# Kernel tuning notes

Hardware: AMD Instinct MI355X
Metric: run time of the kernel (lower is better)

Reference implementation:

```python
import jax, jax.numpy as jnp
import numpy as np

D = 128          # embedding dim
N_INIT = 100000  # number of initial (axiom) clauses
L = 64           # topological levels of derived clauses
M = 4096         # derived clauses per level
N_THAX = 2000    # distinct axiom-name (thax) embeddings
N_SINE = 32      # sine-level embeddings
N_RULES = 256    # distinct inference rules (each with its own 2-ary MLP)
N_TOT = N_INIT + L * M


def setup_inputs() -> dict:
    key = jax.random.key(0)
    ks = jax.random.split(key, 10)
    rng = np.random.default_rng(0)
    # parents of level-l nodes point to any node created strictly earlier
    parents = np.stack(
        [rng.integers(0, N_INIT + l * M, size=(M, 2)) for l in range(L)]
    ).astype(np.int32)  # [L, M, 2]
    return {
        "thax_table": jax.random.normal(ks[0], (N_THAX, D), jnp.float32) * 0.1,
        "sine_table": jax.random.normal(ks[1], (N_SINE, D), jnp.float32) * 0.1,
        "rule_W": jax.random.normal(ks[2], (N_RULES, 2 * D, D), jnp.float32) * (1.0 / np.sqrt(2 * D)),
        "rule_b": jax.random.normal(ks[3], (N_RULES, D), jnp.float32) * 0.01,
        "eval_w": jax.random.normal(ks[4], (D,), jnp.float32) * (1.0 / np.sqrt(D)),
        "eval_b": jax.random.normal(ks[5], (1,), jnp.float32) * 0.01,
        "pos_vals": jax.random.uniform(ks[6], (N_TOT,), jnp.float32, 0.01, 1.0),
        "neg_vals": jax.random.uniform(ks[7], (N_TOT,), jnp.float32, 0.01, 1.0),
        "init_thax": jax.random.randint(ks[8], (N_INIT,), 0, N_THAX, jnp.int32),
        "init_sine": jax.random.randint(ks[9], (N_INIT,), 0, N_SINE, jnp.int32),
        "parents": jnp.asarray(parents),
        "rules": jnp.asarray(rng.integers(0, N_RULES, size=(L, M)).astype(np.int32)),
    }


def reference(thax_table, sine_table, rule_W, rule_b, eval_w, eval_b,
              pos_vals, neg_vals, init_thax, init_sine, parents, rules):
    n_init = init_thax.shape[0]
    n_lvl, m = rules.shape
    d = thax_table.shape[1]

    # init nodes: embed = init_embeds[thax]() + sine_embedder(sine)
    init_emb = thax_table[init_thax] + sine_table[init_sine]  # [N_INIT, D]
    store0 = jnp.concatenate(
        [init_emb, jnp.zeros((n_lvl * m, d), init_emb.dtype)], axis=0)  # [N_TOT, D]

    # deriv nodes, level by level: gather 2 parents, per-rule MLP (cat -> Linear -> ReLU)
    def step(store, xs):
        lvl, par, rul = xs                       # par: [M,2] int, rul: [M] int
        pe = store[par].reshape(m, 2 * d)        # gather parent embeddings
        emb = jax.nn.relu(jnp.einsum('mi,mio->mo', pe, rule_W[rul]) + rule_b[rul])
        store = jax.lax.dynamic_update_slice(store, emb, (n_init + lvl * m, 0))
        return store, None

    store, _ = jax.lax.scan(step, store0, (jnp.arange(n_lvl), parents, rules))

    # eval_net + weighted BCEWithLogits (pos_weight = tot_neg / tot_pos)
    logits = store @ eval_w + eval_b[0]          # [N_TOT]
    tot = pos_vals + neg_vals
    y = pos_vals / tot
    pw = jnp.sum(neg_vals) / jnp.sum(pos_vals)
    per_node = pw * y * jax.nn.softplus(-logits) + (1.0 - y) * jax.nn.softplus(logits)
    loss = jnp.sum(tot * per_node).reshape(1)
    posOK = jnp.sum(jnp.where(logits >= 0.0, pos_vals, 0.0))
    negOK = jnp.sum(jnp.where(logits < 0.0, neg_vals, 0.0))
    return (loss, posOK, negOK)
```

## Files before the change

### kernel.cpp

```cpp
#include <hip/hip_runtime.h>

#define D      128
#define NINIT  100000
#define LVLS   64
#define M      4096
#define NRULES 256
#define NTOT   (NINIT + LVLS * M)
#define NTHR   512
#define TILE   32

typedef __attribute__((ext_vector_type(8))) short short8;
typedef __attribute__((ext_vector_type(4))) float floatx4;

#define ST_OFF 256
#define SI_OFF (ST_OFF + (size_t)NTOT * D * 2)
#define RO_OFF (SI_OFF + (size_t)LVLS * M * 4)
#define FL_OFF (RO_OFF + (size_t)LVLS * (NRULES + 1) * 4)

#define CBAR() asm volatile("" ::: "memory")

__device__ __forceinline__ unsigned short f2bf(float x) {
  unsigned u = __float_as_uint(x);
  u += 0x7fffu + ((u >> 16) & 1u);
  return (unsigned short)(u >> 16);
}

__device__ __forceinline__ float softplusf(float x) {
  return fmaxf(x, 0.f) + log1pf(expf(-fabsf(x)));
}

__device__ __forceinline__ void st_sys(unsigned* p, unsigned v) {
  __hip_atomic_store(p, v, __ATOMIC_RELAXED, __HIP_MEMORY_SCOPE_SYSTEM);
}
__device__ __forceinline__ void st_sys64(unsigned long long* p,
                                         unsigned long long v) {
  __hip_atomic_store(p, v, __ATOMIC_RELAXED, __HIP_MEMORY_SCOPE_SYSTEM);
}
__device__ __forceinline__ unsigned ld_sys(const unsigned* p) {
  return __hip_atomic_load(p, __ATOMIC_RELAXED, __HIP_MEMORY_SCOPE_SYSTEM);
}
__device__ __forceinline__ void wait_flag(const unsigned* f) {
  int guard = 1 << 17;
  while (__builtin_expect(ld_sys(f) == 0u, 0) && --guard)
    __builtin_amdgcn_s_sleep(1);
  CBAR();
}

__device__ __forceinline__ void gbar_light(unsigned* bcnt, unsigned* bgen) {
  __syncthreads();
  if (threadIdx.x == 0) {
    unsigned g = ld_sys(bgen);
    unsigned v = __hip_atomic_fetch_add(bcnt, 1u, __ATOMIC_RELAXED,
                                        __HIP_MEMORY_SCOPE_SYSTEM);
    if (v == gridDim.x - 1) {
      st_sys(bcnt, 0u);
      st_sys(bgen, g + 1u);
    } else {
      int guard = 1 << 22;
      while (ld_sys(bgen) == g && --guard) __builtin_amdgcn_s_sleep(2);
    }
  }
  __syncthreads();
}

__device__ __forceinline__ bool adv_cursor(int r, const int* __restrict__ ro,
                                           int& l, int& t0, int& off, int& cnt) {
  t0 += TILE;
  while (t0 >= cnt) {
    if (++l >= LVLS) return false;
    off = ro[l * (NRULES + 1) + r];
    cnt = ro[l * (NRULES + 1) + r + 1] - off;
    t0 = 0;
  }
  return true;
}

__global__ __launch_bounds__(NTHR, 2) void fused_kernel(
    const float* __restrict__ thax_table, const float* __restrict__ sine_table,
    const float* __restrict__ rule_W, const float* __restrict__ rule_b,
    const float* __restrict__ eval_w, const float* __restrict__ eval_b,
    const float* __restrict__ pos, const float* __restrict__ neg,
    const int* __restrict__ init_thax, const int* __restrict__ init_sine,
    const int* __restrict__ parents,
    const int* __restrict__ rules,
    unsigned short* __restrict__ store, int* __restrict__ sorted_idx,
    int* __restrict__ rule_off, unsigned* __restrict__ flags,
    float* __restrict__ sums, unsigned* __restrict__ bvars,
    float* __restrict__ out) {
  __shared__ unsigned short pe[TILE * 264];
  __shared__ unsigned short ot[TILE * 136];
  __shared__ int s_sid[2][TILE];
  __shared__ int s_cnt[NRULES];
  __shared__ int s_base[NRULES + 1];
  __shared__ float racc[4];

  unsigned* bcnt = bvars;
  unsigned* bgen = bvars + 1;

  const int r = blockIdx.x;
  const int tid = threadIdx.x;
  const int wave = tid >> 6, lane = tid & 63;
  const int col = (wave << 4) + (lane & 15);
  const int node = tid >> 4;
  const int segq = tid & 15;
  const int gid = r * NTHR + tid;
  const int gthreads = NRULES * NTHR;

  float aP1 = 0.f, aP2 = 0.f, a_pos = 0.f, a_neg = 0.f;
  const float eb = eval_b[0];
  float w8[8];
  {
    float4 wA = ((const float4*)eval_w)[segq * 2];
    float4 wB = ((const float4*)eval_w)[segq * 2 + 1];
    w8[0] = wA.x; w8[1] = wA.y; w8[2] = wA.z; w8[3] = wA.w;
    w8[4] = wB.x; w8[5] = wB.y; w8[6] = wB.z; w8[7] = wB.w;
  }

  short8 bf[8];
  {
    const float* Wr = rule_W + (size_t)r * (2 * D * D);
    const int krow_base = (lane >> 4) * 8;
#pragma unroll
    for (int ks = 0; ks < 8; ++ks) {
      union { short8 s; unsigned short us[8]; } c;
#pragma unroll
      for (int j = 0; j < 8; ++j)
        c.us[j] = f2bf(Wr[(size_t)(ks * 32 + krow_base + j) * D + col]);
      bf[ks] = c.s;
    }
  }
  const float bias = rule_b[r * D + col];

  if (r < LVLS) {
    const int l = r;
    const int* rl = rules + (size_t)l * M;
    if (tid < NRULES) s_cnt[tid] = 0;
    __syncthreads();
    for (int m = tid; m < M; m += NTHR) atomicAdd(&s_cnt[rl[m]], 1);
    __syncthreads();
    if (tid == 0) {
      int run = 0;
      for (int q = 0; q < NRULES; ++q) { s_base[q] = run; run += s_cnt[q]; }
      s_base[NRULES] = run;
    }
    __syncthreads();
    if (tid < NRULES) {
      st_sys((unsigned*)&rule_off[(size_t)l * (NRULES + 1) + tid],
             (unsigned)s_base[tid]);
      s_cnt[tid] = s_base[tid];
    }
    if (tid == 0)
      st_sys((unsigned*)&rule_off[(size_t)l * (NRULES + 1) + NRULES],
             (unsigned)M);
    __syncthreads();
    for (int m = tid; m < M; m += NTHR) {
      int p = atomicAdd(&s_cnt[rl[m]], 1);
      st_sys((unsigned*)&sorted_idx[(size_t)l * M + p], (unsigned)m);
    }
  }

  for (int idx = gid; idx < NINIT * 16; idx += gthreads) {
    int nd = idx >> 4, sg = idx & 15;
    const float4* t = (const float4*)(thax_table + (size_t)init_thax[nd] * D) + sg * 2;
    const float4* s = (const float4*)(sine_table + (size_t)init_sine[nd] * D) + sg * 2;
    float4 a0 = t[0], a1 = t[1], b0 = s[0], b1 = s[1];
    float v[8] = {a0.x + b0.x, a0.y + b0.y, a0.z + b0.z, a0.w + b0.w,
                  a1.x + b1.x, a1.y + b1.y, a1.z + b1.z, a1.w + b1.w};
    unsigned p0 = (unsigned)f2bf(v[0]) | ((unsigned)f2bf(v[1]) << 16);
    unsigned p1 = (unsigned)f2bf(v[2]) | ((unsigned)f2bf(v[3]) << 16);
    unsigned p2 = (unsigned)f2bf(v[4]) | ((unsigned)f2bf(v[5]) << 16);
    unsigned p3 = (unsigned)f2bf(v[6]) | ((unsigned)f2bf(v[7]) << 16);
    unsigned long long* dst =
        (unsigned long long*)(store + (size_t)nd * D + sg * 8);
    st_sys64(dst + 0, (unsigned long long)p0 | ((unsigned long long)p1 << 32));
    st_sys64(dst + 1, (unsigned long long)p2 | ((unsigned long long)p3 << 32));

    float pd = v[0] * w8[0] + v[1] * w8[1] + v[2] * w8[2] + v[3] * w8[3] +
               v[4] * w8[4] + v[5] * w8[5] + v[6] * w8[6] + v[7] * w8[7];
    pd += __shfl_xor(pd, 1, 64);
    pd += __shfl_xor(pd, 2, 64);
    pd += __shfl_xor(pd, 4, 64);
    pd += __shfl_xor(pd, 8, 64);
    if (sg == 0) {
      float logit = pd + eb;
      float pp = pos[nd], nn = neg[nd];
      float tot = pp + nn, y = pp / tot;
      aP1 += tot * y * softplusf(-logit);
      aP2 += tot * (1.f - y) * softplusf(logit);
      if (logit >= 0.f) a_pos += pp; else a_neg += nn;
    }
  }

  {
    float sp = 0.f, sn = 0.f;
    for (int i = gid; i < NTOT; i += gthreads) {
      sp += pos[i];
      sn += neg[i];
    }
    for (int m = 32; m; m >>= 1) {
      sp += __shfl_xor(sp, m, 64);
      sn += __shfl_xor(sn, m, 64);
    }
    if (lane == 0) {
      atomicAdd(&sums[0], sp);
      atomicAdd(&sums[1], sn);
    }
  }

  gbar_light(bcnt, bgen);

  const float pw = sums[1] / sums[0];

  int lL = -1, t0L = 0, offL = 0, cntL = 0;

  bool validA = adv_cursor(r, rule_off, lL, t0L, offL, cntL);
  int lA = lL, t0A = t0L, cntA = cntL;
  int parA0 = 0, parA1 = 0;
  bool lateA0 = false, lateA1 = false;
  unsigned reA0 = 1u, reA1 = 1u;
  float pPosA = 0.f, pNegA = 0.f;
  uint4 gA0 = {0, 0, 0, 0}, gA1 = {0, 0, 0, 0};
  if (validA) {
    int gj = t0A + node; if (gj > cntA - 1) gj = cntA - 1;
    int sid = sorted_idx[(size_t)lA * M + offL + gj];
    parA0 = parents[((size_t)lA * M + sid) * 2 + 0];
    parA1 = parents[((size_t)lA * M + sid) * 2 + 1];
    pPosA = pos[NINIT + lA * M + sid];
    pNegA = neg[NINIT + lA * M + sid];
    if (parA0 >= NINIT) wait_flag(flags + (parA0 - NINIT));
    if (parA1 >= NINIT) wait_flag(flags + (parA1 - NINIT));
    gA0 = *(const uint4*)(store + (size_t)parA0 * D + segq * 8);
    gA1 = *(const uint4*)(store + (size_t)parA1 * D + segq * 8);
    if (segq == 0) s_sid[0][node] = sid;
  }

  bool validB = validA && adv_cursor(r, rule_off, lL, t0L, offL, cntL);
  int lB = lL, t0B = t0L, cntB = cntL;
  int sidB = 0, parB0 = 0, parB1 = 0;
  unsigned fB0 = 1u, fB1 = 1u;
  if (validB) {
    int gj = t0B + node; if (gj > cntB - 1) gj = cntB - 1;
    sidB = sorted_idx[(size_t)lB * M + offL + gj];
    parB0 = parents[((size_t)lB * M + sidB) * 2 + 0];
    parB1 = parents[((size_t)lB * M + sidB) * 2 + 1];
    fB0 = parB0 >= NINIT ? ld_sys(flags + (parB0 - NINIT)) : 1u;
    fB1 = parB1 >= NINIT ? ld_sys(flags + (parB1 - NINIT)) : 1u;
  }

  bool validC = validB && adv_cursor(r, rule_off, lL, t0L, offL, cntL);
  int lC = lL, t0C = t0L, cntC = cntL;
  int sidC = 0, parC0 = 0, parC1 = 0;
  if (validC) {
    int gj = t0C + node; if (gj > cntC - 1) gj = cntC - 1;
    sidC = sorted_idx[(size_t)lC * M + offL + gj];
    parC0 = parents[((size_t)lC * M + sidC) * 2 + 0];
    parC1 = parents[((size_t)lC * M + sidC) * 2 + 1];
  }

  bool validD = validC && adv_cursor(r, rule_off, lL, t0L, offL, cntL);
  int lD = lL, t0D = t0L, offD = offL, cntD = cntL;

  int p = 0;
  while (validA) {
    if (lateA0 || lateA1) {
      bool n0 = lateA0 && (reA0 == 0u);
      bool n1 = lateA1 && (reA1 == 0u);
      if (n0 || n1) {
        int guard = 1 << 17;
        while (guard--) {
          unsigned f0 = n0 ? ld_sys(flags + (parA0 - NINIT)) : 1u;
          unsigned f1 = n1 ? ld_sys(flags + (parA1 - NINIT)) : 1u;
          if (f0 != 0u && f1 != 0u) break;
          __builtin_amdgcn_s_sleep(1);
        }
      }
      CBAR();
      if (lateA0) gA0 = *(const uint4*)(store + (size_t)parA0 * D + segq * 8);
      if (lateA1) gA1 = *(const uint4*)(store + (size_t)parA1 * D + segq * 8);
    }

    *(uint4*)(pe + node * 264 + segq * 8) = gA0;
    *(uint4*)(pe + node * 264 + 128 + segq * 8) = gA1;
    __syncthreads();
    if (validB && segq == 0) s_sid[p ^ 1][node] = sidB;

    floatx4 acc0 = {0.f, 0.f, 0.f, 0.f}, acc1 = {0.f, 0.f, 0.f, 0.f};
#pragma unroll
    for (int ks = 0; ks < 8; ++ks) {
      short8 a0 = *(const short8*)(pe + (lane & 15) * 264 + ks * 32 + (lane >> 4) * 8);
      short8 a1 = *(const short8*)(pe + (16 + (lane & 15)) * 264 + ks * 32 + (lane >> 4) * 8);
      acc0 = __builtin_amdgcn_mfma_f32_16x16x32_bf16(a0, bf[ks], acc0, 0, 0, 0);
      acc1 = __builtin_amdgcn_mfma_f32_16x16x32_bf16(a1, bf[ks], acc1, 0, 0, 0);
    }
#pragma unroll
    for (int reg = 0; reg < 4; ++reg) {
      int row = (lane >> 4) * 4 + reg;
      float v0 = acc0[reg] + bias;
      float v1 = acc1[reg] + bias;
      ot[row * 136 + col] = f2bf(v0 > 0.f ? v0 : 0.f);
      ot[(16 + row) * 136 + col] = f2bf(v1 > 0.f ? v1 : 0.f);
    }
    __syncthreads();

    {
      const int n_baseA = NINIT + lA * M;
      int nsid[4]; bool inr[4]; int S = 0;
#pragma unroll
      for (int k = 0; k < 4; ++k) {
        int nd = wave + 8 * k;
        nsid[k] = s_sid[p][nd];
        inr[k] = (t0A + nd) < cntA;
        if (inr[k]) {
          st_sys((unsigned*)(store + (size_t)(n_baseA + nsid[k]) * D) + lane,
                 *(const unsigned*)(ot + nd * 136 + lane * 2));
          ++S;
        }
      }
      CBAR();
#pragma unroll
      for (int k = 0; k < 4; ++k) {
        if (inr[k]) {
          if (S == 4)      asm volatile("s_waitcnt vmcnt(3)" ::: "memory");
          else if (S == 3) asm volatile("s_waitcnt vmcnt(2)" ::: "memory");
          else if (S == 2) asm volatile("s_waitcnt vmcnt(1)" ::: "memory");
          else             asm volatile("s_waitcnt vmcnt(0)" ::: "memory");
          if (lane == 0) st_sys(flags + lA * M + nsid[k], 1u);
        }
      }
      CBAR();
    }

    bool lateB0 = validB && parB0 >= NINIT && fB0 == 0u;
    bool lateB1 = validB && parB1 >= NINIT && fB1 == 0u;
    uint4 gB0, gB1;
    {
      const unsigned short* a0 =
          (validB && !lateB0) ? store + (size_t)parB0 * D : store;
      const unsigned short* a1 =
          (validB && !lateB1) ? store + (size_t)parB1 * D : store;
      gB0 = *(const uint4*)(a0 + segq * 8);
      gB1 = *(const uint4*)(a1 + segq * 8);
    }
    float pPosB = 0.f, pNegB = 0.f;
    if (validB) {
      pPosB = pos[NINIT + lB * M + sidB];
      pNegB = neg[NINIT + lB * M + sidB];
    }
    int sidD = 0, parD0 = 0, parD1 = 0;
    if (validD) {
      int gj = t0D + node; if (gj > cntD - 1) gj = cntD - 1;
      sidD = sorted_idx[(size_t)lD * M + offD + gj];
      parD0 = parents[((size_t)lD * M + sidD) * 2 + 0];
      parD1 = parents[((size_t)lD * M + sidD) * 2 + 1];
    }
    unsigned fC0 = 1u, fC1 = 1u;
    if (validC) {
      fC0 = ld_sys(flags + (parC0 >= NINIT ? parC0 - NINIT : 0));
      fC1 = ld_sys(flags + (parC1 >= NINIT ? parC1 - NINIT : 0));
      if (parC0 < NINIT) fC0 = 1u;
      if (parC1 < NINIT) fC1 = 1u;
    }
    unsigned reB0 = 1u, reB1 = 1u;
    if (lateB0) reB0 = ld_sys(flags + (parB0 - NINIT));
    if (lateB1) reB1 = ld_sys(flags + (parB1 - NINIT));
    CBAR();

    {
      const uint4 u = *(const uint4*)(ot + node * 136 + segq * 8);
      float pd = __uint_as_float(u.x << 16) * w8[0] +
                 __uint_as_float(u.x & 0xffff0000u) * w8[1] +
                 __uint_as_float(u.y << 16) * w8[2] +
                 __uint_as_float(u.y & 0xffff0000u) * w8[3] +
                 __uint_as_float(u.z << 16) * w8[4] +
                 __uint_as_float(u.z & 0xffff0000u) * w8[5] +
                 __uint_as_float(u.w << 16) * w8[6] +
                 __uint_as_float(u.w & 0xffff0000u) * w8[7];
      pd += __shfl_xor(pd, 1, 64);
      pd += __shfl_xor(pd, 2, 64);
      pd += __shfl_xor(pd, 4, 64);
      pd += __shfl_xor(pd, 8, 64);
      if (segq == 0 && (t0A + node) < cntA) {
        float logit = pd + eb;
        float tot = pPosA + pNegA, y = pPosA / tot;
        aP1 += tot * y * softplusf(-logit);
        aP2 += tot * (1.f - y) * softplusf(logit);
        if (logit >= 0.f) a_pos += pPosA; else a_neg += pNegA;
      }
    }

    gA0 = gB0; gA1 = gB1; lateA0 = lateB0; lateA1 = lateB1;
    reA0 = reB0; reA1 = reB1;
    parA0 = parB0; parA1 = parB1;
    pPosA = pPosB; pNegA = pNegB;
    lA = lB; t0A = t0B; cntA = cntB; validA = validB;
    sidB = sidC; parB0 = parC0; parB1 = parC1; fB0 = fC0; fB1 = fC1;
    lB = lC; t0B = t0C; cntB = cntC; validB = validC;
    sidC = sidD; parC0 = parD0; parC1 = parD1;
    lC = lD; t0C = t0D; cntC = cntD; validC = validD;
    validD = validC && adv_cursor(r, rule_off, lL, t0L, offL, cntL);
    lD = lL; t0D = t0L; offD = offL; cntD = cntL;
    p ^= 1;
  }

  for (int m = 32; m; m >>= 1) {
    aP1   += __shfl_xor(aP1,   m, 64);
    aP2   += __shfl_xor(aP2,   m, 64);
    a_pos += __shfl_xor(a_pos, m, 64);
    a_neg += __shfl_xor(a_neg, m, 64);
  }
  if (tid == 0) { racc[0] = 0.f; racc[1] = 0.f; racc[2] = 0.f; racc[3] = 0.f; }
  __syncthreads();
  if (lane == 0) {
    atomicAdd(&racc[0], aP1);
    atomicAdd(&racc[1], aP2);
    atomicAdd(&racc[2], a_pos);
    atomicAdd(&racc[3], a_neg);
  }
  __syncthreads();
  if (tid == 0) {
    atomicAdd(&out[0], pw * racc[0] + racc[1]);
    atomicAdd(&out[1], racc[2]);
    atomicAdd(&out[2], racc[3]);
  }
}

extern "C" void kernel_launch(void* const* d_in, const int* in_sizes, int n_in,
                              void* d_out, int out_size, void* d_ws, size_t ws_size,
                              hipStream_t stream) {
  const float* thax_table = (const float*)d_in[0];
  const float* sine_table = (const float*)d_in[1];
  const float* rule_W     = (const float*)d_in[2];
  const float* rule_b     = (const float*)d_in[3];
  const float* eval_w     = (const float*)d_in[4];
  const float* eval_b     = (const float*)d_in[5];
  const float* pos_vals   = (const float*)d_in[6];
  const float* neg_vals   = (const float*)d_in[7];
  const int*   init_thax  = (const int*)d_in[8];
  const int*   init_sine  = (const int*)d_in[9];
  const int*   parents    = (const int*)d_in[10];
  const int*   rules      = (const int*)d_in[11];

  float* out = (float*)d_out;
  char* ws = (char*)d_ws;
  float* sums = (float*)ws;
  unsigned* bvars = (unsigned*)(ws + 128);
  unsigned short* store = (unsigned short*)(ws + ST_OFF);
  int* sorted_idx = (int*)(ws + SI_OFF);
  int* rule_off   = (int*)(ws + RO_OFF);
  unsigned* flags = (unsigned*)(ws + FL_OFF);

  (void)hipMemsetAsync(d_out, 0, 3 * sizeof(float), stream);
  (void)hipMemsetAsync(d_ws, 0, 256, stream);
  (void)hipMemsetAsync(ws + FL_OFF, 0, (size_t)LVLS * M * 4, stream);

  void* args[] = {&thax_table, &sine_table, &rule_W, &rule_b, &eval_w, &eval_b,
                  &pos_vals, &neg_vals, &init_thax, &init_sine, &parents,
                  &rules, &store, &sorted_idx, &rule_off, &flags, &sums,
                  &bvars, &out};
  (void)hipLaunchCooperativeKernel((void*)fused_kernel, dim3(NRULES),
                                   dim3(NTHR), args, 0, stream);
}
```

Measured before the change: 419.8 us.

## Deepen software pipeline, batch flag waits, parallel scan, split init work off level blocks

Lengthens the per-block prefetch pipeline by one stage so sorted indices, parents, pos/neg values and flag polls are issued further ahead. Flag publication is deferred until after the eval dot product, using a single vmcnt wait, instead of being interleaved with per-store waits. Spin waits now poll both parent flags together with wave-wide __all checks and no sleep. The serial rule-count prefix sum becomes a parallel scan, and init-embedding and pos/neg sum work is moved to the blocks that do not sort levels. The goal is to hide gather and flag latency on the dependent level chain, at the cost of more registers and busier polling.

```diff
diff --git a/kernel.cpp b/kernel.cpp
--- a/kernel.cpp
+++ b/kernel.cpp
@@ -39,10 +39,20 @@
 __device__ __forceinline__ unsigned ld_sys(const unsigned* p) {
   return __hip_atomic_load(p, __ATOMIC_RELAXED, __HIP_MEMORY_SCOPE_SYSTEM);
 }
-__device__ __forceinline__ void wait_flag(const unsigned* f) {
-  int guard = 1 << 17;
-  while (__builtin_expect(ld_sys(f) == 0u, 0) && --guard)
-    __builtin_amdgcn_s_sleep(1);
+
+__device__ __forceinline__ void wait2(const unsigned* f0, bool n0,
+                                      const unsigned* f1, bool n1) {
+  if (__all(!(n0 || n1))) return;
+  unsigned a0 = ld_sys(f0), a1 = ld_sys(f1);
+  int guard = 1 << 16;
+  for (;;) {
+    unsigned b0 = ld_sys(f0), b1 = ld_sys(f1);
+    bool ok = (!n0 || a0 != 0u) && (!n1 || a1 != 0u);
+    if (__all(ok) || !--guard) break;
+    a0 = ld_sys(f0); a1 = ld_sys(f1);
+    ok = (!n0 || b0 != 0u) && (!n1 || b1 != 0u);
+    if (__all(ok) || !--guard) break;
+  }
   CBAR();
 }
 
@@ -103,8 +113,6 @@
   const int col = (wave << 4) + (lane & 15);
   const int node = tid >> 4;
   const int segq = tid & 15;
-  const int gid = r * NTHR + tid;
-  const int gthreads = NRULES * NTHR;
 
   float aP1 = 0.f, aP2 = 0.f, a_pos = 0.f, a_neg = 0.f;
   const float eb = eval_b[0];
@@ -138,16 +146,20 @@
     __syncthreads();
     for (int m = tid; m < M; m += NTHR) atomicAdd(&s_cnt[rl[m]], 1);
     __syncthreads();
-    if (tid == 0) {
-      int run = 0;
-      for (int q = 0; q < NRULES; ++q) { s_base[q] = run; run += s_cnt[q]; }
-      s_base[NRULES] = run;
-    }
-    __syncthreads();
+    int c = (tid < NRULES) ? s_cnt[tid] : 0;
+    if (tid < NRULES) s_base[tid] = c;
+    __syncthreads();
+    for (int off = 1; off < NRULES; off <<= 1) {
+      int t = (tid < NRULES && tid >= off) ? s_base[tid - off] : 0;
+      __syncthreads();
+      if (tid < NRULES) s_base[tid] += t;
+      __syncthreads();
+    }
     if (tid < NRULES) {
+      int ex = s_base[tid] - c;
       st_sys((unsigned*)&rule_off[(size_t)l * (NRULES + 1) + tid],
-             (unsigned)s_base[tid]);
-      s_cnt[tid] = s_base[tid];
+             (unsigned)ex);
+      s_cnt[tid] = ex;
     }
     if (tid == 0)
       st_sys((unsigned*)&rule_off[(size_t)l * (NRULES + 1) + NRULES],
@@ -157,43 +169,42 @@
       int p = atomicAdd(&s_cnt[rl[m]], 1);
       st_sys((unsigned*)&sorted_idx[(size_t)l * M + p], (unsigned)m);
     }
-  }
-
-  for (int idx = gid; idx < NINIT * 16; idx += gthreads) {
-    int nd = idx >> 4, sg = idx & 15;
-    const float4* t = (const float4*)(thax_table + (size_t)init_thax[nd] * D) + sg * 2;
-    const float4* s = (const float4*)(sine_table + (size_t)init_sine[nd] * D) + sg * 2;
-    float4 a0 = t[0], a1 = t[1], b0 = s[0], b1 = s[1];
-    float v[8] = {a0.x + b0.x, a0.y + b0.y, a0.z + b0.z, a0.w + b0.w,
-                  a1.x + b1.x, a1.y + b1.y, a1.z + b1.z, a1.w + b1.w};
-    unsigned p0 = (unsigned)f2bf(v[0]) | ((unsigned)f2bf(v[1]) << 16);
-    unsigned p1 = (unsigned)f2bf(v[2]) | ((unsigned)f2bf(v[3]) << 16);
-    unsigned p2 = (unsigned)f2bf(v[4]) | ((unsigned)f2bf(v[5]) << 16);
-    unsigned p3 = (unsigned)f2bf(v[6]) | ((unsigned)f2bf(v[7]) << 16);
-    unsigned long long* dst =
-        (unsigned long long*)(store + (size_t)nd * D + sg * 8);
-    st_sys64(dst + 0, (unsigned long long)p0 | ((unsigned long long)p1 << 32));
-    st_sys64(dst + 1, (unsigned long long)p2 | ((unsigned long long)p3 << 32));
-
-    float pd = v[0] * w8[0] + v[1] * w8[1] + v[2] * w8[2] + v[3] * w8[3] +
-               v[4] * w8[4] + v[5] * w8[5] + v[6] * w8[6] + v[7] * w8[7];
-    pd += __shfl_xor(pd, 1, 64);
-    pd += __shfl_xor(pd, 2, 64);
-    pd += __shfl_xor(pd, 4, 64);
-    pd += __shfl_xor(pd, 8, 64);
-    if (sg == 0) {
-      float logit = pd + eb;
-      float pp = pos[nd], nn = neg[nd];
-      float tot = pp + nn, y = pp / tot;
-      aP1 += tot * y * softplusf(-logit);
-      aP2 += tot * (1.f - y) * softplusf(logit);
-      if (logit >= 0.f) a_pos += pp; else a_neg += nn;
-    }
-  }
-
-  {
+  } else {
+    const int gid3 = (r - LVLS) * NTHR + tid;
+    const int gstride3 = (NRULES - LVLS) * NTHR;
+    for (int idx = gid3; idx < NINIT * 16; idx += gstride3) {
+      int nd = idx >> 4, sg = idx & 15;
+      const float4* t = (const float4*)(thax_table + (size_t)init_thax[nd] * D) + sg * 2;
+      const float4* s = (const float4*)(sine_table + (size_t)init_sine[nd] * D) + sg * 2;
+      float4 a0 = t[0], a1 = t[1], b0 = s[0], b1 = s[1];
+      float v[8] = {a0.x + b0.x, a0.y + b0.y, a0.z + b0.z, a0.w + b0.w,
+                    a1.x + b1.x, a1.y + b1.y, a1.z + b1.z, a1.w + b1.w};
+      unsigned p0 = (unsigned)f2bf(v[0]) | ((unsigned)f2bf(v[1]) << 16);
+      unsigned p1 = (unsigned)f2bf(v[2]) | ((unsigned)f2bf(v[3]) << 16);
+      unsigned p2 = (unsigned)f2bf(v[4]) | ((unsigned)f2bf(v[5]) << 16);
+      unsigned p3 = (unsigned)f2bf(v[6]) | ((unsigned)f2bf(v[7]) << 16);
+      unsigned long long* dst =
+          (unsigned long long*)(store + (size_t)nd * D + sg * 8);
+      st_sys64(dst + 0, (unsigned long long)p0 | ((unsigned long long)p1 << 32));
+      st_sys64(dst + 1, (unsigned long long)p2 | ((unsigned long long)p3 << 32));
+
+      float pd = v[0] * w8[0] + v[1] * w8[1] + v[2] * w8[2] + v[3] * w8[3] +
+                 v[4] * w8[4] + v[5] * w8[5] + v[6] * w8[6] + v[7] * w8[7];
+      pd += __shfl_xor(pd, 1, 64);
+      pd += __shfl_xor(pd, 2, 64);
+      pd += __shfl_xor(pd, 4, 64);
+      pd += __shfl_xor(pd, 8, 64);
+      if (sg == 0) {
+        float logit = pd + eb;
+        float pp = pos[nd], nn = neg[nd];
+        float tot = pp + nn, y = pp / tot;
+        aP1 += tot * y * softplusf(-logit);
+        aP2 += tot * (1.f - y) * softplusf(logit);
+        if (logit >= 0.f) a_pos += pp; else a_neg += nn;
+      }
+    }
     float sp = 0.f, sn = 0.f;
-    for (int i = gid; i < NTOT; i += gthreads) {
+    for (int i = gid3; i < NTOT; i += gstride3) {
       sp += pos[i];
       sn += neg[i];
     }
@@ -227,8 +238,9 @@
     parA1 = parents[((size_t)lA * M + sid) * 2 + 1];
     pPosA = pos[NINIT + lA * M + sid];
     pNegA = neg[NINIT + lA * M + sid];
-    if (parA0 >= NINIT) wait_flag(flags + (parA0 - NINIT));
-    if (parA1 >= NINIT) wait_flag(flags + (parA1 - NINIT));
+    bool n0 = parA0 >= NINIT, n1 = parA1 >= NINIT;
+    wait2(flags + (n0 ? parA0 - NINIT : 0), n0,
+          flags + (n1 ? parA1 - NINIT : 0), n1);
     gA0 = *(const uint4*)(store + (size_t)parA0 * D + segq * 8);
     gA1 = *(const uint4*)(store + (size_t)parA1 * D + segq * 8);
     if (segq == 0) s_sid[0][node] = sid;
@@ -238,6 +250,7 @@
   int lB = lL, t0B = t0L, cntB = cntL;
   int sidB = 0, parB0 = 0, parB1 = 0;
   unsigned fB0 = 1u, fB1 = 1u;
+  float pPosB = 0.f, pNegB = 0.f;
   if (validB) {
     int gj = t0B + node; if (gj > cntB - 1) gj = cntB - 1;
     sidB = sorted_idx[(size_t)lB * M + offL + gj];
@@ -245,6 +258,8 @@
     parB1 = parents[((size_t)lB * M + sidB) * 2 + 1];
     fB0 = parB0 >= NINIT ? ld_sys(flags + (parB0 - NINIT)) : 1u;
     fB1 = parB1 >= NINIT ? ld_sys(flags + (parB1 - NINIT)) : 1u;
+    pPosB = pos[NINIT + lB * M + sidB];
+    pNegB = neg[NINIT + lB * M + sidB];
   }
 
   bool validC = validB && adv_cursor(r, rule_off, lL, t0L, offL, cntL);
@@ -257,24 +272,24 @@
     parC1 = parents[((size_t)lC * M + sidC) * 2 + 1];
   }
 
-  bool validD = validC && adv_cursor(r, rule_off, lL, t0L, offL, cntL);
-  int lD = lL, t0D = t0L, offD = offL, cntD = cntL;
+  bool validE = validC && adv_cursor(r, rule_off, lL, t0L, offL, cntL);
+  int lE = lL, t0E = t0L, cntE = cntL;
+  int sidE = 0;
+  if (validE) {
+    int gj = t0E + node; if (gj > cntE - 1) gj = cntE - 1;
+    sidE = sorted_idx[(size_t)lE * M + offL + gj];
+  }
+
+  bool validF = validE && adv_cursor(r, rule_off, lL, t0L, offL, cntL);
+  int lF = lL, t0F = t0L, offF = offL, cntF = cntL;
 
   int p = 0;
   while (validA) {
-    if (lateA0 || lateA1) {
+    {
       bool n0 = lateA0 && (reA0 == 0u);
       bool n1 = lateA1 && (reA1 == 0u);
-      if (n0 || n1) {
-        int guard = 1 << 17;
-        while (guard--) {
-          unsigned f0 = n0 ? ld_sys(flags + (parA0 - NINIT)) : 1u;
-          unsigned f1 = n1 ? ld_sys(flags + (parA1 - NINIT)) : 1u;
-          if (f0 != 0u && f1 != 0u) break;
-          __builtin_amdgcn_s_sleep(1);
-        }
-      }
-      CBAR();
+      wait2(flags + (lateA0 ? parA0 - NINIT : 0), n0,
+            flags + (lateA1 ? parA1 - NINIT : 0), n1);
       if (lateA0) gA0 = *(const uint4*)(store + (size_t)parA0 * D + segq * 8);
       if (lateA1) gA1 = *(const uint4*)(store + (size_t)parA1 * D + segq * 8);
     }
@@ -302,67 +317,38 @@
     }
     __syncthreads();
 
-    {
-      const int n_baseA = NINIT + lA * M;
-      int nsid[4]; bool inr[4]; int S = 0;
+    const int n_baseA = NINIT + lA * M;
 #pragma unroll
-      for (int k = 0; k < 4; ++k) {
-        int nd = wave + 8 * k;
-        nsid[k] = s_sid[p][nd];
-        inr[k] = (t0A + nd) < cntA;
-        if (inr[k]) {
-          st_sys((unsigned*)(store + (size_t)(n_baseA + nsid[k]) * D) + lane,
-                 *(const unsigned*)(ot + nd * 136 + lane * 2));
-          ++S;
-        }
-      }
-      CBAR();
-#pragma unroll
-      for (int k = 0; k < 4; ++k) {
-        if (inr[k]) {
-          if (S == 4)      asm volatile("s_waitcnt vmcnt(3)" ::: "memory");
-          else if (S == 3) asm volatile("s_waitcnt vmcnt(2)" ::: "memory");
-          else if (S == 2) asm volatile("s_waitcnt vmcnt(1)" ::: "memory");
-          else             asm volatile("s_waitcnt vmcnt(0)" ::: "memory");
-          if (lane == 0) st_sys(flags + lA * M + nsid[k], 1u);
-        }
-      }
-      CBAR();
-    }
+    for (int k = 0; k < 4; ++k) {
+      int nd = wave + 8 * k;
+      if ((t0A + nd) < cntA)
+        st_sys((unsigned*)(store + (size_t)(n_baseA + s_sid[p][nd]) * D) + lane,
+               *(const unsigned*)(ot + nd * 136 + lane * 2));
+    }
+    CBAR();
 
     bool lateB0 = validB && parB0 >= NINIT && fB0 == 0u;
     bool lateB1 = validB && parB1 >= NINIT && fB1 == 0u;
-    uint4 gB0, gB1;
-    {
-      const unsigned short* a0 =
-          (validB && !lateB0) ? store + (size_t)parB0 * D : store;
-      const unsigned short* a1 =
-          (validB && !lateB1) ? store + (size_t)parB1 * D : store;
-      gB0 = *(const uint4*)(a0 + segq * 8);
-      gB1 = *(const uint4*)(a1 + segq * 8);
-    }
-    float pPosB = 0.f, pNegB = 0.f;
-    if (validB) {
-      pPosB = pos[NINIT + lB * M + sidB];
-      pNegB = neg[NINIT + lB * M + sidB];
-    }
-    int sidD = 0, parD0 = 0, parD1 = 0;
-    if (validD) {
-      int gj = t0D + node; if (gj > cntD - 1) gj = cntD - 1;
-      sidD = sorted_idx[(size_t)lD * M + offD + gj];
-      parD0 = parents[((size_t)lD * M + sidD) * 2 + 0];
-      parD1 = parents[((size_t)lD * M + sidD) * 2 + 1];
-    }
-    unsigned fC0 = 1u, fC1 = 1u;
-    if (validC) {
-      fC0 = ld_sys(flags + (parC0 >= NINIT ? parC0 - NINIT : 0));
-      fC1 = ld_sys(flags + (parC1 >= NINIT ? parC1 - NINIT : 0));
-      if (parC0 < NINIT) fC0 = 1u;
-      if (parC1 < NINIT) fC1 = 1u;
-    }
-    unsigned reB0 = 1u, reB1 = 1u;
-    if (lateB0) reB0 = ld_sys(flags + (parB0 - NINIT));
-    if (lateB1) reB1 = ld_sys(flags + (parB1 - NINIT));
+    const unsigned short* ga0 =
+        (validB && !lateB0) ? store + (size_t)parB0 * D : store;
+    const unsigned short* ga1 =
+        (validB && !lateB1) ? store + (size_t)parB1 * D : store;
+    uint4 gB0 = *(const uint4*)(ga0 + segq * 8);
+    uint4 gB1 = *(const uint4*)(ga1 + segq * 8);
+    unsigned pol0 =
+        ld_sys(flags + ((validC && parC0 >= NINIT) ? parC0 - NINIT : 0));
+    unsigned pol1 =
+        ld_sys(flags + ((validC && parC1 >= NINIT) ? parC1 - NINIT : 0));
+    int idxC = NINIT + lC * M + sidC;
+    float posC = pos[validC ? idxC : 0];
+    float negC = neg[validC ? idxC : 0];
+    int2 prE = *(const int2*)(parents +
+                (validE ? (((size_t)lE * M + sidE) * 2) : 0));
+    int cF = cntF > 0 ? cntF : 1;
+    int gjF = t0F + node; if (gjF > cF - 1) gjF = cF - 1; if (gjF < 0) gjF = 0;
+    int sidF = sorted_idx[validF ? ((size_t)lF * M + offF + gjF) : 0];
+    unsigned reB0 = ld_sys(flags + (lateB0 ? parB0 - NINIT : 0));
+    unsigned reB1 = ld_sys(flags + (lateB1 ? parB1 - NINIT : 0));
     CBAR();
 
     {
@@ -388,17 +374,36 @@
       }
     }
 
-    gA0 = gB0; gA1 = gB1; lateA0 = lateB0; lateA1 = lateB1;
+    asm volatile("s_waitcnt vmcnt(10)" ::: "memory");
+    if (lane < 4) {
+      int nd = wave + 8 * lane;
+      int sidw = s_sid[p][nd];
+      if ((t0A + nd) < cntA) st_sys(flags + lA * M + sidw, 1u);
+    }
+    CBAR();
+
+    lateA0 = lateB0; lateA1 = lateB1;
     reA0 = reB0; reA1 = reB1;
+    gA0 = gB0; gA1 = gB1;
     parA0 = parB0; parA1 = parB1;
     pPosA = pPosB; pNegA = pNegB;
     lA = lB; t0A = t0B; cntA = cntB; validA = validB;
-    sidB = sidC; parB0 = parC0; parB1 = parC1; fB0 = fC0; fB1 = fC1;
+
+    parB0 = parC0; parB1 = parC1; sidB = sidC;
+    fB0 = (validC && parC0 >= NINIT) ? pol0 : 1u;
+    fB1 = (validC && parC1 >= NINIT) ? pol1 : 1u;
+    pPosB = posC; pNegB = negC;
     lB = lC; t0B = t0C; cntB = cntC; validB = validC;
-    sidC = sidD; parC0 = parD0; parC1 = parD1;
-    lC = lD; t0C = t0D; cntC = cntD; validC = validD;
-    validD = validC && adv_cursor(r, rule_off, lL, t0L, offL, cntL);
-    lD = lL; t0D = t0L; offD = offL; cntD = cntL;
+
+    parC0 = validE ? prE.x : 0; parC1 = validE ? prE.y : 0;
+    sidC = sidE;
+    lC = lE; t0C = t0E; cntC = cntE; validC = validE;
+
+    sidE = sidF;
+    lE = lF; t0E = t0F; cntE = cntF; validE = validF;
+
+    validF = validF && adv_cursor(r, rule_off, lL, t0L, offL, cntL);
+    lF = lL; t0F = t0L; offF = offL; cntF = cntL;
     p ^= 1;
   }
 
```

Result: faster. 392.5 us (median of 2 runs) (-6.5%).
